# Kernel tuning notes

Hardware: AMD Instinct MI355X
Metric: run time of the kernel (lower is better)

Reference implementation:

```python
import jax, jax.numpy as jnp
import numpy as np

B, S, H = 4, 2048, 576
NH, NKV, HD = 9, 3, 64
GROUPS = NH // NKV
ROPE_THETA = 100000.0
MAX_POS = 8192


def _rope_tables():
    inv_freq = 1.0 / (ROPE_THETA ** (jnp.arange(0, HD, 2, dtype=jnp.float32) / HD))
    t = jnp.arange(MAX_POS, dtype=jnp.float32)
    freqs = jnp.outer(t, inv_freq)              # [MAX_POS, HD//2]
    emb = jnp.concatenate([freqs, freqs], axis=-1)  # [MAX_POS, HD]
    return jnp.cos(emb), jnp.sin(emb)


def _rotate_half(x):
    x1, x2 = x[..., : HD // 2], x[..., HD // 2 :]
    return jnp.concatenate([-x2, x1], axis=-1)


def setup_inputs() -> dict:
    key = jax.random.key(0)
    k1, k2, k3, k4, k5 = jax.random.split(key, 5)
    hidden_states = jax.random.normal(k1, (B, S, H), dtype=jnp.float32)
    # causal additive mask [B,1,S,S]: 0 where allowed, large negative above diagonal
    causal = jnp.triu(jnp.ones((S, S), dtype=bool), k=1)
    attention_mask = jnp.where(causal, jnp.float32(-1e9), jnp.float32(0.0))[None, None]
    attention_mask = jnp.broadcast_to(attention_mask, (B, 1, S, S))
    position_ids = jnp.broadcast_to(jnp.arange(S, dtype=jnp.int32)[None, :], (B, S))
    scale = 1.0 / np.sqrt(H)
    Wq = jax.random.normal(k2, (NH * HD, H), dtype=jnp.float32) * scale
    Wk = jax.random.normal(k3, (NKV * HD, H), dtype=jnp.float32) * scale
    Wv = jax.random.normal(k4, (NKV * HD, H), dtype=jnp.float32) * scale
    Wo = jax.random.normal(k5, (H, NH * HD), dtype=jnp.float32) * scale
    return {"hidden_states": hidden_states, "attention_mask": attention_mask,
            "position_ids": position_ids, "Wq": Wq, "Wk": Wk, "Wv": Wv, "Wo": Wo}


def reference(hidden_states, attention_mask, position_ids, Wq, Wk, Wv, Wo):
    bsz, q_len, _ = hidden_states.shape
    cos_cached, sin_cached = _rope_tables()
    # projections (nn.Linear: x @ W.T), reshape to [B, heads, S, HD]
    q = (hidden_states @ Wq.T).reshape(bsz, q_len, NH, HD).transpose(0, 2, 1, 3)
    k = (hidden_states @ Wk.T).reshape(bsz, q_len, NKV, HD).transpose(0, 2, 1, 3)
    v = (hidden_states @ Wv.T).reshape(bsz, q_len, NKV, HD).transpose(0, 2, 1, 3)
    # RoPE: gather cos/sin per position, broadcast over heads
    cos = cos_cached[position_ids][:, None]  # [B,1,S,HD]
    sin = sin_cached[position_ids][:, None]
    q = q * cos + _rotate_half(q) * sin
    k = k * cos + _rotate_half(k) * sin
    # GQA: repeat_interleave kv heads
    k = jnp.repeat(k, GROUPS, axis=1)  # [B,NH,S,HD]
    v = jnp.repeat(v, GROUPS, axis=1)
    scores = jnp.einsum('bhqd,bhkd->bhqk', q, k) / np.sqrt(HD)
    scores = scores + attention_mask
    probs = jax.nn.softmax(scores.astype(jnp.float32), axis=-1).astype(q.dtype)
    attn = jnp.einsum('bhqk,bhkd->bhqd', probs, v)
    attn = attn.transpose(0, 2, 1, 3).reshape(bsz, q_len, NH * HD)
    return attn @ Wo.T
```

## Files before the change

### kernel.cpp

```cpp
#include <hip/hip_runtime.h>
#include <hip/hip_bf16.h>
#include <math.h>

#define Bsz 4
#define Slen 2048
#define Hdim 576
#define NH 9
#define NKV 3
#define HD 64

typedef __bf16 bf16_t;
typedef __bf16 bf16x8 __attribute__((ext_vector_type(8)));
typedef float f32x4 __attribute__((ext_vector_type(4)));
typedef float f32x16 __attribute__((ext_vector_type(16)));
typedef unsigned int u32;
typedef unsigned int u32x4 __attribute__((ext_vector_type(4)));

static __device__ __forceinline__ bf16x8 load_cvt8(const float* __restrict__ src){
  float4 f0 = *reinterpret_cast<const float4*>(src);
  float4 f1 = *reinterpret_cast<const float4*>(src + 4);
  bf16x8 v;
  v[0]=(bf16_t)f0.x; v[1]=(bf16_t)f0.y; v[2]=(bf16_t)f0.z; v[3]=(bf16_t)f0.w;
  v[4]=(bf16_t)f1.x; v[5]=(bf16_t)f1.y; v[6]=(bf16_t)f1.z; v[7]=(bf16_t)f1.w;
  return v;
}

static __device__ __forceinline__ void gload16(const bf16_t* g, bf16_t* l){
  __builtin_amdgcn_global_load_lds((const __attribute__((address_space(1))) void*)g,
                                   (__attribute__((address_space(3))) void*)l, 16, 0, 0);
}

static __device__ __forceinline__ float xhalf_sum(float x){
  return x + __shfl_xor(x, 32, 64);
}

__global__ void setup_kernel(const float* __restrict__ X,
                             const float* __restrict__ Wq,
                             const float* __restrict__ Wk,
                             const float* __restrict__ Wv,
                             const float* __restrict__ Wo,
                             bf16_t* __restrict__ Xb,
                             bf16_t* __restrict__ Wb,
                             bf16_t* __restrict__ Wob,
                             float* __restrict__ cost,
                             float* __restrict__ sint)
{
  const int bid = blockIdx.x;
  if (bid < 256){
    int i = bid * 256 + threadIdx.x;
    int j = i & 31;
    int p = i >> 5;
    double invf = pow(100000.0, -(double)j / 32.0);
    double ang = (double)p * invf;
    cost[i] = (float)cos(ang);
    sint[i] = (float)sin(ang);
    return;
  }
  const int NX  = 8192 * 576 / 8;
  const int NWq = 576 * 576 / 8;
  const int NWk = 192 * 576 / 8;
  int i = (bid - 256) * 256 + threadIdx.x;
  const int total = NX + NWq + 2 * NWk + NWq;
  if (i >= total) return;
  const float* src; bf16_t* dst; int off;
  if (i < NX)                    { src = X;  dst = Xb;            off = i; }
  else if (i < NX + NWq)         { src = Wq; dst = Wb;            off = i - NX; }
  else if (i < NX + NWq + NWk)   { src = Wk; dst = Wb + 331776;   off = i - NX - NWq; }
  else if (i < NX + NWq + 2*NWk) { src = Wv; dst = Wb + 442368;   off = i - NX - NWq - NWk; }
  else                           { src = Wo; dst = Wob;           off = i - NX - NWq - 2*NWk; }
  *reinterpret_cast<bf16x8*>(dst + (size_t)off * 8) = load_cvt8(src + (size_t)off * 8);
}

__launch_bounds__(256)
__global__ void qkv_gemm_kernel(const bf16_t* __restrict__ Xb,
                                const bf16_t* __restrict__ Wb,
                                const int* __restrict__ pos_ids,
                                const float* __restrict__ cost,
                                const float* __restrict__ sint,
                                float qscale,
                                bf16_t* __restrict__ qbuf,
                                bf16_t* __restrict__ kbuf,
                                bf16_t* __restrict__ vtbuf)
{
  __shared__ bf16_t Ald[2][128 * 64];
  __shared__ bf16_t Bld[2][128 * 64];
  const int t = threadIdx.x, l = t & 63, w = t >> 6;
  const int wm = w >> 1, wn = w & 1;
  const int lane16 = l & 15, grp = l >> 4;
  const int m0 = blockIdx.x * 128;
  const int p  = blockIdx.y;
  const int nrow0 = p * 128;

  const int sr = l >> 3;
  const int sc = ((l & 7) ^ sr) * 8;

  f32x4 acc[4][4];
  #pragma unroll
  for (int mi = 0; mi < 4; ++mi)
    #pragma unroll
    for (int nj = 0; nj < 4; ++nj)
      acc[mi][nj] = (f32x4){0.f, 0.f, 0.f, 0.f};

  auto STAGE = [&](int kt, int buf){
    const int k0 = kt * 64;
    #pragma unroll
    for (int u = 0; u < 4; ++u)
      gload16(Xb + (size_t)(m0 + w * 32 + u * 8 + sr) * Hdim + k0 + sc,
              &Ald[buf][(w * 32 + u * 8) * 64]);
    #pragma unroll
    for (int u = 0; u < 4; ++u){
      int br = nrow0 + w * 32 + u * 8 + sr;
      if (br > 959) br = 959;
      gload16(Wb + (size_t)br * Hdim + k0 + sc,
              &Bld[buf][(w * 32 + u * 8) * 64]);
    }
  };

  STAGE(0, 0);
  asm volatile("s_waitcnt vmcnt(0)" ::: "memory");
  __syncthreads();

  const int sl7 = lane16 & 7;
  for (int kt = 0; kt < 9; ++kt){
    const int buf = kt & 1;
    if (kt + 1 < 9) STAGE(kt + 1, buf ^ 1);
    #pragma unroll
    for (int ks = 0; ks < 2; ++ks){
      bf16x8 a[4], bb[4];
      #pragma unroll
      for (int mi = 0; mi < 4; ++mi){
        int row = wm * 64 + mi * 16 + lane16;
        a[mi] = *reinterpret_cast<const bf16x8*>(&Ald[buf][row * 64 + (((ks * 4 + grp) ^ sl7) * 8)]);
      }
      #pragma unroll
      for (int nj = 0; nj < 4; ++nj){
        int row = wn * 64 + (nj & 1) * 32 + (nj >> 1) * 16 + lane16;
        bb[nj] = *reinterpret_cast<const bf16x8*>(&Bld[buf][row * 64 + (((ks * 4 + grp) ^ sl7) * 8)]);
      }
      #pragma unroll
      for (int mi = 0; mi < 4; ++mi)
        #pragma unroll
        for (int nj = 0; nj < 4; ++nj)
          acc[mi][nj] = __builtin_amdgcn_mfma_f32_16x16x32_bf16(a[mi], bb[nj], acc[mi][nj], 0, 0, 0);
    }
    if (kt + 1 < 9){
      asm volatile("s_waitcnt vmcnt(0)" ::: "memory");
      __syncthreads();
    }
  }

  const int h15 = p * 2 + wn;
  if (h15 < 15){
    #pragma unroll
    for (int mi = 0; mi < 4; ++mi){
      #pragma unroll
      for (int k = 0; k < 2; ++k){
        const int d = k * 16 + lane16;
        #pragma unroll
        for (int j2 = 0; j2 < 4; ++j2){
          int m = m0 + wm * 64 + mi * 16 + grp * 4 + j2;
          int b = m >> 11;
          int s = m & 2047;
          float x0 = acc[mi][2 * k][j2], x1 = acc[mi][2 * k + 1][j2];
          if (h15 < 12){
            int pos = pos_ids[b * Slen + s];
            float c = cost[pos * 32 + d], sn = sint[pos * 32 + d];
            float scale = (h15 < 9) ? qscale : 1.0f;
            float o0 = (x0 * c - x1 * sn) * scale;
            float o1 = (x1 * c + x0 * sn) * scale;
            x0 = o0; x1 = o1;
          }
          if (h15 < 9){
            bf16_t* dst = qbuf + (((size_t)b * NH + h15) * Slen + s) * HD;
            dst[d] = (bf16_t)x0; dst[d + 32] = (bf16_t)x1;
          } else if (h15 < 12){
            bf16_t* dst = kbuf + (((size_t)b * NKV + (h15 - 9)) * Slen + s) * HD;
            dst[d] = (bf16_t)x0; dst[d + 32] = (bf16_t)x1;
          } else {
            bf16_t* dst = vtbuf + ((size_t)b * NKV + (h15 - 12)) * HD * Slen + s;
            dst[(size_t)d * Slen] = (bf16_t)x0; dst[(size_t)(d + 32) * Slen] = (bf16_t)x1;
          }
        }
      }
    }
  }
}

__launch_bounds__(128)
__global__ void flash_attn_kernel(const bf16_t* __restrict__ qbuf,
                                  const bf16_t* __restrict__ kbuf,
                                  const bf16_t* __restrict__ vtbuf,
                                  u32* __restrict__ part_O,
                                  float* __restrict__ part_l)
{
  __shared__ bf16_t Kld[2][32 * 64];
  __shared__ bf16_t Vld[2][64 * 32];
  const int t = threadIdx.x, l = t & 63, w = t >> 6;
  const int l32 = l & 31, hi = l >> 5;

  const int flat = blockIdx.x;
  const int xcd = flat & 7, j = flat >> 3;
  const int g   = (xcd >> 1) * 3 + j % 3;
  const int idx = 2 * (j / 3) + (xcd & 1);
  const int b   = g / 3, kvh = g % 3;
  const int qt  = 31 - idx / 6;
  const int rem = idx % 6;
  const int h   = kvh * 3 + (rem >> 1);
  const int seg = rem & 1;
  const int bh  = b * NH + h;
  const int t0 = seg * (qt + 1);
  const int t1 = t0 + qt + 1;

  const bf16_t* qp = qbuf + ((size_t)b * NH + h) * Slen * HD;
  const bf16_t* kp = kbuf + ((size_t)b * NKV + kvh) * Slen * HD;
  const bf16_t* vp = vtbuf + ((size_t)b * NKV + kvh) * HD * Slen;

  const int krow = l >> 3;
  const int ksc  = ((l & 7) ^ krow) * 8;
  const int vrow = l >> 2;
  const int vsc  = ((l & 3) ^ ((vrow >> 1) & 3)) * 8;

  auto STAGE = [&](int kt, int buf){
    const int k0 = kt * 32;
    #pragma unroll
    for (int u = 0; u < 2; ++u){
      int ub = w * 2 + u;
      gload16(kp + (size_t)(k0 + ub * 8 + krow) * HD + ksc, &Kld[buf][ub * 512]);
    }
    #pragma unroll
    for (int u = 0; u < 2; ++u){
      int ub = w * 2 + u;
      gload16(vp + (size_t)(ub * 16 + vrow) * Slen + k0 + vsc, &Vld[buf][ub * 512]);
    }
  };

  const int q0 = qt * 64 + w * 32;
  bf16x8 aq[4];
  #pragma unroll
  for (int ds = 0; ds < 4; ++ds)
    aq[ds] = *reinterpret_cast<const bf16x8*>(qp + (size_t)(q0 + l32) * HD + ds * 16 + hi * 8);

  STAGE(t0, 0);
  if (t0 + 1 < t1) STAGE(t0 + 1, 1);

  f32x16 acco[2];
  #pragma unroll
  for (int db = 0; db < 2; ++db)
    #pragma unroll
    for (int r = 0; r < 16; ++r) acco[db][r] = 0.f;
  float lhalf = 0.f;

  const int dt = 2 * qt + w;
  for (int kb = t0; kb < t1; ++kb){
    const int cur = (kb - t0) & 1;
    const bool rem1 = (kb + 1 < t1), rem2 = (kb + 2 < t1);

    if (rem1) asm volatile("s_waitcnt vmcnt(6)" ::: "memory");
    else      asm volatile("s_waitcnt vmcnt(2)" ::: "memory");
    __syncthreads();

    u32x4 pa0, pa1;
    if (kb <= dt){
      f32x16 sacc;
      #pragma unroll
      for (int r = 0; r < 16; ++r) sacc[r] = 0.f;
      __builtin_amdgcn_s_setprio(1);
      #pragma unroll
      for (int ds = 0; ds < 4; ++ds){
        bf16x8 ak = *reinterpret_cast<const bf16x8*>(
            &Kld[cur][l32 * 64 + (((ds * 2 + hi) ^ (l32 & 7)) * 8)]);
        sacc = __builtin_amdgcn_mfma_f32_32x32x16_bf16(ak, aq[ds], sacc, 0, 0, 0);
      }
      __builtin_amdgcn_s_setprio(0);

      if (kb == dt){
        #pragma unroll
        for (int r = 0; r < 16; ++r){
          int crow = (r & 3) + 8 * (r >> 2) + 4 * hi;
          if (crow > l32) sacc[r] = -1e30f;
        }
      }

      #pragma unroll
      for (int r = 0; r < 16; ++r)
        sacc[r] = __builtin_amdgcn_exp2f(sacc[r]);
      float s0 = sacc[0] + sacc[1],  s1 = sacc[2] + sacc[3];
      float s2 = sacc[4] + sacc[5],  s3 = sacc[6] + sacc[7];
      float s4 = sacc[8] + sacc[9],  s5 = sacc[10] + sacc[11];
      float s6 = sacc[12] + sacc[13], s7 = sacc[14] + sacc[15];
      s0 += s1; s2 += s3; s4 += s5; s6 += s7;
      lhalf += (s0 + s2) + (s4 + s6);

      u32 wv[8];
      #pragma unroll
      for (int jj = 0; jj < 8; ++jj){
        float lo = sacc[2 * jj], hp = sacc[2 * jj + 1];
        asm("v_cvt_pk_bf16_f32 %0, %1, %2" : "=v"(wv[jj]) : "v"(lo), "v"(hp));
      }
      asm volatile("v_permlane32_swap_b32 %0, %1" : "+v"(wv[0]), "+v"(wv[2]));
      asm volatile("v_permlane32_swap_b32 %0, %1" : "+v"(wv[1]), "+v"(wv[3]));
      asm volatile("v_permlane32_swap_b32 %0, %1" : "+v"(wv[4]), "+v"(wv[6]));
      asm volatile("v_permlane32_swap_b32 %0, %1" : "+v"(wv[5]), "+v"(wv[7]));
      pa0 = (u32x4){wv[0], wv[1], wv[2], wv[3]};
      pa1 = (u32x4){wv[4], wv[5], wv[6], wv[7]};
    }

    if (rem1) asm volatile("s_waitcnt vmcnt(4)" ::: "memory");
    else      asm volatile("s_waitcnt vmcnt(0)" ::: "memory");
    __syncthreads();

    if (kb <= dt){
      __builtin_amdgcn_s_setprio(1);
      #pragma unroll
      for (int ks = 0; ks < 2; ++ks){
        #pragma unroll
        for (int db = 0; db < 2; ++db){
          bf16x8 av = *reinterpret_cast<const bf16x8*>(
              &Vld[cur][(db * 32 + l32) * 32 + (((ks * 2 + hi) ^ ((l32 >> 1) & 3)) * 8)]);
          acco[db] = __builtin_amdgcn_mfma_f32_32x32x16_bf16(
              av, __builtin_bit_cast(bf16x8, ks ? pa1 : pa0), acco[db], 0, 0, 0);
        }
      }
      __builtin_amdgcn_s_setprio(0);
    }

    if (rem2){
      __syncthreads();
      STAGE(kb + 2, cur);
    }
  }

  const float lrun = xhalf_sum(lhalf);

  const int slot = (bh * 32 + qt) * 2 + seg;
  u32* po = part_O + ((size_t)slot * 2 + w) * 1024;
  float* pl = part_l + ((size_t)slot * 2 + w) * 64;
  #pragma unroll
  for (int db = 0; db < 2; ++db){
    #pragma unroll
    for (int jj = 0; jj < 8; ++jj){
      int r = 2 * jj;
      int d = db * 32 + (r & 3) + 8 * (r >> 2) + 4 * hi;
      u32 pw;
      float lo = acco[db][r], hp = acco[db][r + 1];
      asm("v_cvt_pk_bf16_f32 %0, %1, %2" : "=v"(pw) : "v"(lo), "v"(hp));
      po[(d >> 1) * 32 + l32] = pw;
    }
  }
  if (hi == 0) pl[l32] = lrun;
}

__launch_bounds__(128)
__global__ void combine_kernel(const u32* __restrict__ part_O,
                               const float* __restrict__ part_l,
                               bf16_t* __restrict__ attn_out)
{
  const int idx = blockIdx.x;
  const int bh = idx % 36, qt = idx / 36;
  const int b = bh / NH, h = bh % NH;
  const int t = threadIdx.x;
  const int q = t & 31, wg = (t >> 5) & 1, half = t >> 6;
  const int slot0 = (bh * 32 + qt) * 2;

  const float* pl0 = part_l + ((size_t)(slot0 + 0) * 2 + wg) * 64;
  const float* pl1 = part_l + ((size_t)(slot0 + 1) * 2 + wg) * 64;
  float linv = 1.0f / (pl0[q] + pl1[q]);

  const u32* po0 = part_O + ((size_t)(slot0 + 0) * 2 + wg) * 1024;
  const u32* po1 = part_O + ((size_t)(slot0 + 1) * 2 + wg) * 1024;
  const int s = qt * 64 + wg * 32 + q;
  bf16_t* orow = attn_out + ((size_t)b * Slen + s) * (NH * HD) + h * HD;

  #pragma unroll
  for (int u = 0; u < 16; ++u){
    int dp = half * 16 + u;
    u32 v1 = po0[dp * 32 + q], v2 = po1[dp * 32 + q];
    float lo = (__builtin_bit_cast(float, v1 << 16)
              + __builtin_bit_cast(float, v2 << 16)) * linv;
    float hv = (__builtin_bit_cast(float, v1 & 0xffff0000u)
              + __builtin_bit_cast(float, v2 & 0xffff0000u)) * linv;
    u32 pw;
    asm("v_cvt_pk_bf16_f32 %0, %1, %2" : "=v"(pw) : "v"(lo), "v"(hv));
    *reinterpret_cast<u32*>(orow + 2 * dp) = pw;
  }
}

__launch_bounds__(256)
__global__ void out_gemm_kernel(const bf16_t* __restrict__ A,
                                const bf16_t* __restrict__ Wob,
                                float* __restrict__ out)
{
  __shared__ bf16_t Ald[2][128 * 64];
  __shared__ bf16_t Bld[2][64 * 64];
  const int t = threadIdx.x, l = t & 63, w = t >> 6;
  const int wm = w >> 1, wn = w & 1;
  const int lane16 = l & 15, grp = l >> 4;
  const int m0 = blockIdx.x * 128;
  const int nt = blockIdx.y;
  const int nrow0 = nt * 64;

  const int sr = l >> 3;
  const int sc = ((l & 7) ^ sr) * 8;

  f32x4 acc[4][2];
  #pragma unroll
  for (int mi = 0; mi < 4; ++mi)
    #pragma unroll
    for (int ni = 0; ni < 2; ++ni)
      acc[mi][ni] = (f32x4){0.f, 0.f, 0.f, 0.f};

  auto STAGE = [&](int kt, int buf){
    const int k0 = kt * 64;
    #pragma unroll
    for (int u = 0; u < 4; ++u)
      gload16(A + (size_t)(m0 + w * 32 + u * 8 + sr) * Hdim + k0 + sc,
              &Ald[buf][(w * 32 + u * 8) * 64]);
    #pragma unroll
    for (int u = 0; u < 2; ++u)
      gload16(Wob + (size_t)(nrow0 + w * 16 + u * 8 + sr) * Hdim + k0 + sc,
              &Bld[buf][(w * 16 + u * 8) * 64]);
  };

  STAGE(0, 0);
  asm volatile("s_waitcnt vmcnt(0)" ::: "memory");
  __syncthreads();

  const int sl7 = lane16 & 7;
  for (int kt = 0; kt < 9; ++kt){
    const int buf = kt & 1;
    if (kt + 1 < 9) STAGE(kt + 1, buf ^ 1);
    #pragma unroll
    for (int ks = 0; ks < 2; ++ks){
      bf16x8 a[4], bb[2];
      #pragma unroll
      for (int mi = 0; mi < 4; ++mi){
        int row = wm * 64 + mi * 16 + lane16;
        a[mi] = *reinterpret_cast<const bf16x8*>(&Ald[buf][row * 64 + (((ks * 4 + grp) ^ sl7) * 8)]);
      }
      #pragma unroll
      for (int ni = 0; ni < 2; ++ni){
        int row = wn * 32 + ni * 16 + lane16;
        bb[ni] = *reinterpret_cast<const bf16x8*>(&Bld[buf][row * 64 + (((ks * 4 + grp) ^ sl7) * 8)]);
      }
      #pragma unroll
      for (int mi = 0; mi < 4; ++mi)
        #pragma unroll
        for (int ni = 0; ni < 2; ++ni)
          acc[mi][ni] = __builtin_amdgcn_mfma_f32_16x16x32_bf16(a[mi], bb[ni], acc[mi][ni], 0, 0, 0);
    }
    if (kt + 1 < 9){
      asm volatile("s_waitcnt vmcnt(0)" ::: "memory");
      __syncthreads();
    }
  }

  #pragma unroll
  for (int mi = 0; mi < 4; ++mi){
    #pragma unroll
    for (int ni = 0; ni < 2; ++ni){
      #pragma unroll
      for (int jj = 0; jj < 4; ++jj){
        int m = m0 + wm * 64 + mi * 16 + grp * 4 + jj;
        int n = nrow0 + wn * 32 + ni * 16 + lane16;
        out[(size_t)m * Hdim + n] = acc[mi][ni][jj];
      }
    }
  }
}

extern "C" void kernel_launch(void* const* d_in, const int* in_sizes, int n_in,
                              void* d_out, int out_size, void* d_ws, size_t ws_size,
                              hipStream_t stream) {
  const float* X   = (const float*)d_in[0];
  const int* pos   = (const int*)d_in[2];
  const float* Wq  = (const float*)d_in[3];
  const float* Wk  = (const float*)d_in[4];
  const float* Wv  = (const float*)d_in[5];
  const float* Wo  = (const float*)d_in[6];
  float* out = (float*)d_out;

  char* ws = (char*)d_ws;
  float* cost = (float*)ws;
  float* sint = (float*)(ws + 262144);
  bf16_t* qb  = (bf16_t*)(ws + 524288);
  bf16_t* kb  = qb + (size_t)Bsz * NH * Slen * HD;
  bf16_t* vt  = kb + (size_t)Bsz * NKV * Slen * HD;
  bf16_t* Xb  = vt + (size_t)Bsz * NKV * Slen * HD;
  bf16_t* ab  = Xb;
  bf16_t* Wb  = Xb + (size_t)8192 * 576;
  bf16_t* Wob = Wb + (size_t)960 * 576;
  u32*  part_O  = (u32*)(Wob + (size_t)576 * 576);
  float* part_l = (float*)(part_O + (size_t)2304 * 2 * 1024);

  const float QSCALE = 0.125f * 1.44269504088896f;

  setup_kernel<<<dim3(256 + 2736), dim3(256), 0, stream>>>(X, Wq, Wk, Wv, Wo, Xb, Wb, Wob, cost, sint);
  qkv_gemm_kernel<<<dim3(64, 8), dim3(256), 0, stream>>>(Xb, Wb, pos, cost, sint, QSCALE, qb, kb, vt);
  flash_attn_kernel<<<dim3(2304), dim3(128), 0, stream>>>(qb, kb, vt, part_O, part_l);
  combine_kernel<<<dim3(1152), dim3(128), 0, stream>>>(part_O, part_l, ab);
  out_gemm_kernel<<<dim3(64, 9), dim3(256), 0, stream>>>(ab, Wob, out);
}
```

Baseline: 104.7 us.

## Use atomic work-queue persistent scheduling for flash attention tiles

Replaces the static blockIdx-to-tile mapping in the attention kernel with a dynamic scheduler. Each block takes tiles from a global atomic counter, largest query tiles first, and loops until all 2304 work items are done. The counter is reset in the setup kernel. This aims to balance the uneven causal workloads across CUs. In exchange it gives up the XCD-aware mapping that kept blocks sharing a KV head on the same L2, and adds an atomic plus a barrier per tile.

Result: slower. 151.3 us (+44.5%).

```diff
diff --git a/kernel.cpp b/kernel.cpp
--- a/kernel.cpp
+++ b/kernel.cpp
@@ -43,9 +43,11 @@
                              bf16_t* __restrict__ Wb,
                              bf16_t* __restrict__ Wob,
                              float* __restrict__ cost,
-                             float* __restrict__ sint)
+                             float* __restrict__ sint,
+                             int* __restrict__ cnt)
 {
   const int bid = blockIdx.x;
+  if (bid == 0 && threadIdx.x == 0) *cnt = 0;
   if (bid < 256){
     int i = bid * 256 + threadIdx.x;
     int j = i & 31;
@@ -191,163 +193,169 @@
                                   const bf16_t* __restrict__ kbuf,
                                   const bf16_t* __restrict__ vtbuf,
                                   u32* __restrict__ part_O,
-                                  float* __restrict__ part_l)
+                                  float* __restrict__ part_l,
+                                  int* __restrict__ cnt)
 {
   __shared__ bf16_t Kld[2][32 * 64];
   __shared__ bf16_t Vld[2][64 * 32];
+  __shared__ int s_u;
   const int t = threadIdx.x, l = t & 63, w = t >> 6;
   const int l32 = l & 31, hi = l >> 5;
-
-  const int flat = blockIdx.x;
-  const int xcd = flat & 7, j = flat >> 3;
-  const int g   = (xcd >> 1) * 3 + j % 3;
-  const int idx = 2 * (j / 3) + (xcd & 1);
-  const int b   = g / 3, kvh = g % 3;
-  const int qt  = 31 - idx / 6;
-  const int rem = idx % 6;
-  const int h   = kvh * 3 + (rem >> 1);
-  const int seg = rem & 1;
-  const int bh  = b * NH + h;
-  const int t0 = seg * (qt + 1);
-  const int t1 = t0 + qt + 1;
-
-  const bf16_t* qp = qbuf + ((size_t)b * NH + h) * Slen * HD;
-  const bf16_t* kp = kbuf + ((size_t)b * NKV + kvh) * Slen * HD;
-  const bf16_t* vp = vtbuf + ((size_t)b * NKV + kvh) * HD * Slen;
 
   const int krow = l >> 3;
   const int ksc  = ((l & 7) ^ krow) * 8;
   const int vrow = l >> 2;
   const int vsc  = ((l & 3) ^ ((vrow >> 1) & 3)) * 8;
 
-  auto STAGE = [&](int kt, int buf){
-    const int k0 = kt * 32;
-    #pragma unroll
-    for (int u = 0; u < 2; ++u){
-      int ub = w * 2 + u;
-      gload16(kp + (size_t)(k0 + ub * 8 + krow) * HD + ksc, &Kld[buf][ub * 512]);
-    }
-    #pragma unroll
-    for (int u = 0; u < 2; ++u){
-      int ub = w * 2 + u;
-      gload16(vp + (size_t)(ub * 16 + vrow) * Slen + k0 + vsc, &Vld[buf][ub * 512]);
-    }
-  };
-
-  const int q0 = qt * 64 + w * 32;
-  bf16x8 aq[4];
-  #pragma unroll
-  for (int ds = 0; ds < 4; ++ds)
-    aq[ds] = *reinterpret_cast<const bf16x8*>(qp + (size_t)(q0 + l32) * HD + ds * 16 + hi * 8);
-
-  STAGE(t0, 0);
-  if (t0 + 1 < t1) STAGE(t0 + 1, 1);
-
-  f32x16 acco[2];
-  #pragma unroll
-  for (int db = 0; db < 2; ++db)
-    #pragma unroll
-    for (int r = 0; r < 16; ++r) acco[db][r] = 0.f;
-  float lhalf = 0.f;
-
-  const int dt = 2 * qt + w;
-  for (int kb = t0; kb < t1; ++kb){
-    const int cur = (kb - t0) & 1;
-    const bool rem1 = (kb + 1 < t1), rem2 = (kb + 2 < t1);
-
-    if (rem1) asm volatile("s_waitcnt vmcnt(6)" ::: "memory");
-    else      asm volatile("s_waitcnt vmcnt(2)" ::: "memory");
+  for (;;){
+    if (t == 0) s_u = atomicAdd(cnt, 1);
     __syncthreads();
-
-    u32x4 pa0, pa1;
-    if (kb <= dt){
-      f32x16 sacc;
-      #pragma unroll
-      for (int r = 0; r < 16; ++r) sacc[r] = 0.f;
-      __builtin_amdgcn_s_setprio(1);
-      #pragma unroll
-      for (int ds = 0; ds < 4; ++ds){
-        bf16x8 ak = *reinterpret_cast<const bf16x8*>(
-            &Kld[cur][l32 * 64 + (((ds * 2 + hi) ^ (l32 & 7)) * 8)]);
-        sacc = __builtin_amdgcn_mfma_f32_32x32x16_bf16(ak, aq[ds], sacc, 0, 0, 0);
-      }
-      __builtin_amdgcn_s_setprio(0);
-
-      if (kb == dt){
-        #pragma unroll
-        for (int r = 0; r < 16; ++r){
-          int crow = (r & 3) + 8 * (r >> 2) + 4 * hi;
-          if (crow > l32) sacc[r] = -1e30f;
+    const int u = s_u;
+    if (u >= 2304) return;
+
+    const int qt  = 31 - u / 72;
+    const int r72 = u % 72;
+    const int seg = r72 / 36;
+    const int bh  = r72 % 36;
+    const int b = bh / NH, h = bh % NH, kvh = h / (NH / NKV);
+    const int t0 = seg * (qt + 1);
+    const int t1 = t0 + qt + 1;
+
+    const bf16_t* qp = qbuf + ((size_t)b * NH + h) * Slen * HD;
+    const bf16_t* kp = kbuf + ((size_t)b * NKV + kvh) * Slen * HD;
+    const bf16_t* vp = vtbuf + ((size_t)b * NKV + kvh) * HD * Slen;
+
+    auto STAGE = [&](int kt, int buf){
+      const int k0 = kt * 32;
+      #pragma unroll
+      for (int uu = 0; uu < 2; ++uu){
+        int ub = w * 2 + uu;
+        gload16(kp + (size_t)(k0 + ub * 8 + krow) * HD + ksc, &Kld[buf][ub * 512]);
+      }
+      #pragma unroll
+      for (int uu = 0; uu < 2; ++uu){
+        int ub = w * 2 + uu;
+        gload16(vp + (size_t)(ub * 16 + vrow) * Slen + k0 + vsc, &Vld[buf][ub * 512]);
+      }
+    };
+
+    const int q0 = qt * 64 + w * 32;
+    bf16x8 aq[4];
+    #pragma unroll
+    for (int ds = 0; ds < 4; ++ds)
+      aq[ds] = *reinterpret_cast<const bf16x8*>(qp + (size_t)(q0 + l32) * HD + ds * 16 + hi * 8);
+
+    STAGE(t0, 0);
+    if (t0 + 1 < t1) STAGE(t0 + 1, 1);
+
+    f32x16 acco[2];
+    #pragma unroll
+    for (int db = 0; db < 2; ++db)
+      #pragma unroll
+      for (int r = 0; r < 16; ++r) acco[db][r] = 0.f;
+    float lhalf = 0.f;
+
+    const int dt = 2 * qt + w;
+    for (int kb = t0; kb < t1; ++kb){
+      const int cur = (kb - t0) & 1;
+      const bool rem1 = (kb + 1 < t1), rem2 = (kb + 2 < t1);
+
+      if (rem1) asm volatile("s_waitcnt vmcnt(6)" ::: "memory");
+      else      asm volatile("s_waitcnt vmcnt(2)" ::: "memory");
+      __syncthreads();
+
+      u32x4 pa0, pa1;
+      if (kb <= dt){
+        f32x16 sacc;
+        #pragma unroll
+        for (int r = 0; r < 16; ++r) sacc[r] = 0.f;
+        __builtin_amdgcn_s_setprio(1);
+        #pragma unroll
+        for (int ds = 0; ds < 4; ++ds){
+          bf16x8 ak = *reinterpret_cast<const bf16x8*>(
+              &Kld[cur][l32 * 64 + (((ds * 2 + hi) ^ (l32 & 7)) * 8)]);
+          sacc = __builtin_amdgcn_mfma_f32_32x32x16_bf16(ak, aq[ds], sacc, 0, 0, 0);
         }
-      }
-
-      #pragma unroll
-      for (int r = 0; r < 16; ++r)
-        sacc[r] = __builtin_amdgcn_exp2f(sacc[r]);
-      float s0 = sacc[0] + sacc[1],  s1 = sacc[2] + sacc[3];
-      float s2 = sacc[4] + sacc[5],  s3 = sacc[6] + sacc[7];
-      float s4 = sacc[8] + sacc[9],  s5 = sacc[10] + sacc[11];
-      float s6 = sacc[12] + sacc[13], s7 = sacc[14] + sacc[15];
-      s0 += s1; s2 += s3; s4 += s5; s6 += s7;
-      lhalf += (s0 + s2) + (s4 + s6);
-
-      u32 wv[8];
+        __builtin_amdgcn_s_setprio(0);
+
+        if (kb == dt){
+          #pragma unroll
+          for (int r = 0; r < 16; ++r){
+            int crow = (r & 3) + 8 * (r >> 2) + 4 * hi;
+            if (crow > l32) sacc[r] = -1e30f;
+          }
+        }
+
+        #pragma unroll
+        for (int r = 0; r < 16; ++r)
+          sacc[r] = __builtin_amdgcn_exp2f(sacc[r]);
+        float s0 = sacc[0] + sacc[1],  s1 = sacc[2] + sacc[3];
+        float s2 = sacc[4] + sacc[5],  s3 = sacc[6] + sacc[7];
+        float s4 = sacc[8] + sacc[9],  s5 = sacc[10] + sacc[11];
+        float s6 = sacc[12] + sacc[13], s7 = sacc[14] + sacc[15];
+        s0 += s1; s2 += s3; s4 += s5; s6 += s7;
+        lhalf += (s0 + s2) + (s4 + s6);
+
+        u32 wv[8];
+        #pragma unroll
+        for (int jj = 0; jj < 8; ++jj){
+          float lo = sacc[2 * jj], hp = sacc[2 * jj + 1];
+          asm("v_cvt_pk_bf16_f32 %0, %1, %2" : "=v"(wv[jj]) : "v"(lo), "v"(hp));
+        }
+        asm volatile("v_permlane32_swap_b32 %0, %1" : "+v"(wv[0]), "+v"(wv[2]));
+        asm volatile("v_permlane32_swap_b32 %0, %1" : "+v"(wv[1]), "+v"(wv[3]));
+        asm volatile("v_permlane32_swap_b32 %0, %1" : "+v"(wv[4]), "+v"(wv[6]));
+        asm volatile("v_permlane32_swap_b32 %0, %1" : "+v"(wv[5]), "+v"(wv[7]));
+        pa0 = (u32x4){wv[0], wv[1], wv[2], wv[3]};
+        pa1 = (u32x4){wv[4], wv[5], wv[6], wv[7]};
+      }
+
+      if (rem1) asm volatile("s_waitcnt vmcnt(4)" ::: "memory");
+      else      asm volatile("s_waitcnt vmcnt(0)" ::: "memory");
+      __syncthreads();
+
+      if (kb <= dt){
+        __builtin_amdgcn_s_setprio(1);
+        #pragma unroll
+        for (int ks = 0; ks < 2; ++ks){
+          #pragma unroll
+          for (int db = 0; db < 2; ++db){
+            bf16x8 av = *reinterpret_cast<const bf16x8*>(
+                &Vld[cur][(db * 32 + l32) * 32 + (((ks * 2 + hi) ^ ((l32 >> 1) & 3)) * 8)]);
+            acco[db] = __builtin_amdgcn_mfma_f32_32x32x16_bf16(
+                av, __builtin_bit_cast(bf16x8, ks ? pa1 : pa0), acco[db], 0, 0, 0);
+          }
+        }
+        __builtin_amdgcn_s_setprio(0);
+      }
+
+      if (rem2){
+        __syncthreads();
+        STAGE(kb + 2, cur);
+      }
+    }
+
+    const float lrun = xhalf_sum(lhalf);
+
+    const int slot = (bh * 32 + qt) * 2 + seg;
+    u32* po = part_O + ((size_t)slot * 2 + w) * 1024;
+    float* pl = part_l + ((size_t)slot * 2 + w) * 64;
+    #pragma unroll
+    for (int db = 0; db < 2; ++db){
       #pragma unroll
       for (int jj = 0; jj < 8; ++jj){
-        float lo = sacc[2 * jj], hp = sacc[2 * jj + 1];
-        asm("v_cvt_pk_bf16_f32 %0, %1, %2" : "=v"(wv[jj]) : "v"(lo), "v"(hp));
-      }
-      asm volatile("v_permlane32_swap_b32 %0, %1" : "+v"(wv[0]), "+v"(wv[2]));
-      asm volatile("v_permlane32_swap_b32 %0, %1" : "+v"(wv[1]), "+v"(wv[3]));
-      asm volatile("v_permlane32_swap_b32 %0, %1" : "+v"(wv[4]), "+v"(wv[6]));
-      asm volatile("v_permlane32_swap_b32 %0, %1" : "+v"(wv[5]), "+v"(wv[7]));
-      pa0 = (u32x4){wv[0], wv[1], wv[2], wv[3]};
-      pa1 = (u32x4){wv[4], wv[5], wv[6], wv[7]};
-    }
-
-    if (rem1) asm volatile("s_waitcnt vmcnt(4)" ::: "memory");
-    else      asm volatile("s_waitcnt vmcnt(0)" ::: "memory");
+        int r = 2 * jj;
+        int d = db * 32 + (r & 3) + 8 * (r >> 2) + 4 * hi;
+        u32 pw;
+        float lo = acco[db][r], hp = acco[db][r + 1];
+        asm("v_cvt_pk_bf16_f32 %0, %1, %2" : "=v"(pw) : "v"(lo), "v"(hp));
+        po[(d >> 1) * 32 + l32] = pw;
+      }
+    }
+    if (hi == 0) pl[l32] = lrun;
+
     __syncthreads();
-
-    if (kb <= dt){
-      __builtin_amdgcn_s_setprio(1);
-      #pragma unroll
-      for (int ks = 0; ks < 2; ++ks){
-        #pragma unroll
-        for (int db = 0; db < 2; ++db){
-          bf16x8 av = *reinterpret_cast<const bf16x8*>(
-              &Vld[cur][(db * 32 + l32) * 32 + (((ks * 2 + hi) ^ ((l32 >> 1) & 3)) * 8)]);
-          acco[db] = __builtin_amdgcn_mfma_f32_32x32x16_bf16(
-              av, __builtin_bit_cast(bf16x8, ks ? pa1 : pa0), acco[db], 0, 0, 0);
-        }
-      }
-      __builtin_amdgcn_s_setprio(0);
-    }
-
-    if (rem2){
-      __syncthreads();
-      STAGE(kb + 2, cur);
-    }
-  }
-
-  const float lrun = xhalf_sum(lhalf);
-
-  const int slot = (bh * 32 + qt) * 2 + seg;
-  u32* po = part_O + ((size_t)slot * 2 + w) * 1024;
-  float* pl = part_l + ((size_t)slot * 2 + w) * 64;
-  #pragma unroll
-  for (int db = 0; db < 2; ++db){
-    #pragma unroll
-    for (int jj = 0; jj < 8; ++jj){
-      int r = 2 * jj;
-      int d = db * 32 + (r & 3) + 8 * (r >> 2) + 4 * hi;
-      u32 pw;
-      float lo = acco[db][r], hp = acco[db][r + 1];
-      asm("v_cvt_pk_bf16_f32 %0, %1, %2" : "=v"(pw) : "v"(lo), "v"(hp));
-      po[(d >> 1) * 32 + l32] = pw;
-    }
-  }
-  if (hi == 0) pl[l32] = lrun;
+  }
 }
 
 __launch_bounds__(128)
@@ -491,12 +499,13 @@
   bf16_t* Wob = Wb + (size_t)960 * 576;
   u32*  part_O  = (u32*)(Wob + (size_t)576 * 576);
   float* part_l = (float*)(part_O + (size_t)2304 * 2 * 1024);
+  int*  cnt     = (int*)(part_l + (size_t)2304 * 2 * 64);
 
   const float QSCALE = 0.125f * 1.44269504088896f;
 
-  setup_kernel<<<dim3(256 + 2736), dim3(256), 0, stream>>>(X, Wq, Wk, Wv, Wo, Xb, Wb, Wob, cost, sint);
+  setup_kernel<<<dim3(256 + 2736), dim3(256), 0, stream>>>(X, Wq, Wk, Wv, Wo, Xb, Wb, Wob, cost, sint, cnt);
   qkv_gemm_kernel<<<dim3(64, 8), dim3(256), 0, stream>>>(Xb, Wb, pos, cost, sint, QSCALE, qb, kb, vt);
-  flash_attn_kernel<<<dim3(2304), dim3(128), 0, stream>>>(qb, kb, vt, part_O, part_l);
+  flash_attn_kernel<<<dim3(2560), dim3(128), 0, stream>>>(qb, kb, vt, part_O, part_l, cnt);
   combine_kernel<<<dim3(1152), dim3(128), 0, stream>>>(part_O, part_l, ab);
   out_gemm_kernel<<<dim3(64, 9), dim3(256), 0, stream>>>(ab, Wob, out);
 }
```
